# Kernel tuning notes

Measured on AMD Instinct MI355X. Metric: run time of the kernel, lower is better.

## Reference

```python
import jax, jax.numpy as jnp
import numpy as np

UNITS = 256


def setup_inputs() -> dict:
    key = jax.random.key(0)
    ks = jax.random.split(key, 9)
    B, H, W, C = 8, 64, 64, UNITS
    x = jax.random.normal(ks[0], (B, H, W, C), dtype=jnp.float32)
    # 1x1 Conv2D == per-pixel linear: weight [C_in, C_out], bias [C_out]
    def lin(k):
        return jax.random.normal(k, (C, UNITS), dtype=jnp.float32) * (2.0 / C) ** 0.5
    return {
        "x": x,
        "wq": lin(ks[1]), "bq": jnp.zeros((UNITS,), jnp.float32),
        "wk": lin(ks[2]), "bk": jnp.zeros((UNITS,), jnp.float32),
        "wv": lin(ks[3]), "bv": jnp.zeros((UNITS,), jnp.float32),
        "wp": lin(ks[4]), "bp": jnp.zeros((UNITS,), jnp.float32),
    }


def reference(x, wq, bq, wk, bk, wv, bv, wp, bp):
    B, H, W, C = x.shape
    N = H * W
    scale = jnp.asarray(UNITS, jnp.float32) ** -0.5
    xf = x.reshape(B, N, C)  # 1x1 conv == matmul over channels
    q = xf @ wq + bq
    k = xf @ wk + bk
    v = xf @ wv + bv
    # (b,h,w,c)x(b,H,W,c)->(b,h,w,H,W) flattened to (b,N,N)
    scores = jnp.einsum('bnc,bmc->bnm', q, k) * scale
    attn = jax.nn.softmax(scores, axis=-1)
    out = jnp.einsum('bnm,bmc->bnc', attn, v)
    proj = out @ wp + bp
    return x + proj.reshape(B, H, W, UNITS)
```

## Files before the change

### kernel.cpp

```cpp
#include <hip/hip_runtime.h>


typedef _Float16 half8 __attribute__((ext_vector_type(8)));
typedef _Float16 half4 __attribute__((ext_vector_type(4)));
typedef float f32x4 __attribute__((ext_vector_type(4)));
typedef float f32x16 __attribute__((ext_vector_type(16)));
typedef unsigned int u32x4 __attribute__((ext_vector_type(4)));
typedef unsigned int u32x2 __attribute__((ext_vector_type(2)));

#define MFMA16(a, b, c) __builtin_amdgcn_mfma_f32_16x16x32_f16((a), (b), (c), 0, 0, 0)
#define MFMA32(a, b, c) __builtin_amdgcn_mfma_f32_32x32x16_f16((a), (b), (c), 0, 0, 0)

#if __has_builtin(__builtin_amdgcn_exp2f)
#define EXP2(x) __builtin_amdgcn_exp2f(x)
#else
#define EXP2(x) exp2f(x)
#endif

#define QSCALE 0.09016843898f
#define ESHIFT 11.5415603f

__device__ __forceinline__ void lds_load16(const void* g, void* l) {
    __builtin_amdgcn_global_load_lds(
        (const __attribute__((address_space(1))) unsigned int*)g,
        (__attribute__((address_space(3))) unsigned int*)l, 16, 0, 0);
}

__global__ __launch_bounds__(256)
void wt_prep(const float* __restrict__ w0, const float* __restrict__ w1,
             const float* __restrict__ w2, const float* __restrict__ w3,
             _Float16* __restrict__ outw)
{
    __shared__ _Float16 sT[64 * 72];
    const int z = blockIdx.z;
    const float* W = (z == 0) ? w0 : (z == 1) ? w1 : (z == 2) ? w2 : w3;
    _Float16* O = outw + z * 65536;
    const int kb = blockIdx.x * 64, nb = blockIdx.y * 64;
    const int t = threadIdx.x;
    const int r = t >> 4, c4 = (t & 15) * 4;
#pragma unroll
    for (int i = 0; i < 4; ++i) {
        f32x4 ld = *(const f32x4*)(W + (size_t)(kb + r + i * 16) * 256 + nb + c4);
#pragma unroll
        for (int j = 0; j < 4; ++j) sT[(c4 + j) * 72 + r + i * 16] = (_Float16)ld[j];
    }
    __syncthreads();
#pragma unroll
    for (int i = 0; i < 4; ++i) {
        int n = r + i * 16;
        *(u32x2*)&O[(size_t)(nb + n) * 256 + kb + c4] = *(const u32x2*)&sT[n * 72 + c4];
    }
}

__global__ __launch_bounds__(256)
void qkv_gemm(const float* __restrict__ x, const _Float16* __restrict__ wt,
              const float* __restrict__ bq, const float* __restrict__ bk,
              const float* __restrict__ bv,
              _Float16* __restrict__ qo, _Float16* __restrict__ ko,
              _Float16* __restrict__ vo)
{
    __shared__ _Float16 smem[4 * 2560];
    _Float16* sA = smem;

    const int tid  = threadIdx.x;
    const int w    = tid >> 6;
    const int lane = tid & 63;
    const int quad = lane >> 4;
    const int l16  = lane & 15;
    const int m0   = blockIdx.x * 64;
    const int n0   = blockIdx.y * 64;
    const int rS = tid >> 2, cS = (tid & 3) << 3;

    const float* ap = x + (size_t)(m0 + rS) * 256 + cS;
    f32x4 a0 = *(const f32x4*)ap, a1 = *(const f32x4*)(ap + 4);
    u32x4 bst[3];
#pragma unroll
    for (int o = 0; o < 3; ++o)
        bst[o] = *(const u32x4*)(wt + o * 65536 + (size_t)(n0 + rS) * 256 + cS);

    f32x4 zero4 = {0.f, 0.f, 0.f, 0.f};
    f32x4 acc[3][4];
#pragma unroll
    for (int o = 0; o < 3; ++o)
#pragma unroll
        for (int mt = 0; mt < 4; ++mt) acc[o][mt] = zero4;

    for (int it = 0; it < 8; ++it) {
        __syncthreads();
        half8 t;
#pragma unroll
        for (int j = 0; j < 4; ++j) { t[j] = (_Float16)a0[j]; t[j + 4] = (_Float16)a1[j]; }
        *(half8*)&sA[rS * 40 + cS] = t;
#pragma unroll
        for (int o = 0; o < 3; ++o)
            *(u32x4*)&smem[2560 * (o + 1) + rS * 40 + cS] = bst[o];
        __syncthreads();
        if (it < 7) {
            int k0 = (it + 1) * 32;
            const float* ap2 = x + (size_t)(m0 + rS) * 256 + k0 + cS;
            a0 = *(const f32x4*)ap2; a1 = *(const f32x4*)(ap2 + 4);
#pragma unroll
            for (int o = 0; o < 3; ++o)
                bst[o] = *(const u32x4*)(wt + o * 65536 + (size_t)(n0 + rS) * 256 + k0 + cS);
        }
        half8 af[4];
#pragma unroll
        for (int mt = 0; mt < 4; ++mt)
            af[mt] = *(const half8*)&sA[(mt * 16 + l16) * 40 + quad * 8];
#pragma unroll
        for (int o = 0; o < 3; ++o) {
            half8 bf = *(const half8*)&smem[2560 * (o + 1) + (16 * w + l16) * 40 + quad * 8];
#pragma unroll
            for (int mt = 0; mt < 4; ++mt)
                acc[o][mt] = MFMA16(af[mt], bf, acc[o][mt]);
        }
    }

    const int col = n0 + 16 * w + l16;
#pragma unroll
    for (int mt = 0; mt < 4; ++mt) {
#pragma unroll
        for (int reg = 0; reg < 4; ++reg) {
            int row = m0 + 16 * mt + quad * 4 + reg;
            qo[(size_t)row * 256 + col] = (_Float16)((acc[0][mt][reg] + bq[col]) * QSCALE);
            ko[(size_t)row * 256 + col] = (_Float16)(acc[1][mt][reg] + bk[col]);
        }
    }
    __syncthreads();
    _Float16* sT = smem;
#pragma unroll
    for (int mt = 0; mt < 4; ++mt)
#pragma unroll
        for (int reg = 0; reg < 4; ++reg)
            sT[(16 * w + l16) * 72 + 16 * mt + quad * 4 + reg] =
                (_Float16)(acc[2][mt][reg] + bv[col]);
    __syncthreads();
    int ch = tid >> 2, po = (tid & 3) << 4;
    int bb = m0 >> 12, pix = m0 & 4095;
    _Float16* dst = vo + (size_t)bb * 1048576 + (size_t)(n0 + ch) * 4096 + pix + po;
    *(u32x4*)dst       = *(const u32x4*)&sT[ch * 72 + po];
    *(u32x4*)(dst + 8) = *(const u32x4*)&sT[ch * 72 + po + 8];
}

__global__ __launch_bounds__(256)
void proj_gemm(const _Float16* __restrict__ opart, const float* __restrict__ lpart,
               const _Float16* __restrict__ Wt, const float* __restrict__ bias,
               const float* __restrict__ resid, float* __restrict__ out)
{
    __shared__ _Float16 smem[2 * 2560];
    _Float16* sA = smem;
    _Float16* sB = smem + 2560;

    const int tid  = threadIdx.x;
    const int w    = tid >> 6;
    const int lane = tid & 63;
    const int quad = lane >> 4;
    const int l16  = lane & 15;
    const int m0   = blockIdx.x * 64;
    const int n0   = blockIdx.y * 64;
    const int rS = tid >> 2, cS = (tid & 3) << 3;

    const _Float16* o1p = opart;
    const _Float16* o2p = opart + 8388608;
    const int row = m0 + rS;
    const float inv = 1.0f / (lpart[row] + lpart[32768 + row]);

    u32x4 a1v = *(const u32x4*)(o1p + (size_t)row * 256 + cS);
    u32x4 a2v = *(const u32x4*)(o2p + (size_t)row * 256 + cS);
    u32x4 bst = *(const u32x4*)(Wt + (size_t)(n0 + rS) * 256 + cS);

    f32x4 zero4 = {0.f, 0.f, 0.f, 0.f};
    f32x4 acc[4] = {zero4, zero4, zero4, zero4};

    for (int it = 0; it < 8; ++it) {
        __syncthreads();
        {
            half8 h1 = *(half8*)&a1v, h2 = *(half8*)&a2v, t;
#pragma unroll
            for (int j = 0; j < 8; ++j)
                t[j] = (_Float16)(((float)h1[j] + (float)h2[j]) * inv);
            *(half8*)&sA[rS * 40 + cS] = t;
        }
        *(u32x4*)&sB[rS * 40 + cS] = bst;
        __syncthreads();
        if (it < 7) {
            int k0 = (it + 1) * 32;
            a1v = *(const u32x4*)(o1p + (size_t)row * 256 + k0 + cS);
            a2v = *(const u32x4*)(o2p + (size_t)row * 256 + k0 + cS);
            bst = *(const u32x4*)(Wt + (size_t)(n0 + rS) * 256 + k0 + cS);
        }
        half8 af = *(const half8*)&sA[(16 * w + l16) * 40 + quad * 8];
#pragma unroll
        for (int nt = 0; nt < 4; ++nt) {
            half8 bf = *(const half8*)&sB[(nt * 16 + l16) * 40 + quad * 8];
            acc[nt] = MFMA16(af, bf, acc[nt]);
        }
    }
#pragma unroll
    for (int nt = 0; nt < 4; ++nt) {
#pragma unroll
        for (int reg = 0; reg < 4; ++reg) {
            int orow = m0 + 16 * w + quad * 4 + reg;
            int col = n0 + nt * 16 + l16;
            out[(size_t)orow * 256 + col] =
                acc[nt][reg] + bias[col] + resid[(size_t)orow * 256 + col];
        }
    }
}

__global__ __launch_bounds__(256, 1)
void attn_kernel(const _Float16* __restrict__ q, const _Float16* __restrict__ k,
                 const _Float16* __restrict__ vt, _Float16* __restrict__ opart,
                 float* __restrict__ lpart)
{
    extern __shared__ char smem[];
    char* sKb = smem;
    char* sVb = smem + 32768;

    const int tid  = threadIdx.x;
    const int w    = tid >> 6;
    const int lane = tid & 63;
    const int l31  = lane & 31;
    const int hi   = lane >> 5;
    const int kh   = blockIdx.x & 1;
    const int qg   = (blockIdx.x >> 1) & 15;
    const int b    = blockIdx.x >> 5;

    char* sPw = smem + 65536 + w * 5120;

    const _Float16* kb = k  + (size_t)b * 1048576 + (size_t)kh * 524288;
    const _Float16* vb = vt + (size_t)b * 1048576 + kh * 2048;
    const int rowbase = qg * 256 + w * 64;

    half8 qf0[16], qf1[16];
    {
        const _Float16* q0 = q + (size_t)(b * 4096 + rowbase + l31) * 256 + hi * 8;
        const _Float16* q1 = q0 + 32 * 256;
#pragma unroll
        for (int s = 0; s < 16; ++s) {
            qf0[s] = *(const half8*)(q0 + s * 16);
            qf1[s] = *(const half8*)(q1 + s * 16);
        }
    }

    f32x16 o0[8], o1[8];
#pragma unroll
    for (int i = 0; i < 8; ++i)
#pragma unroll
        for (int j = 0; j < 16; ++j) { o0[i][j] = 0.f; o1[i][j] = 0.f; }
    float ls0 = 0.f, ls1 = 0.f;

    const int koffL = l31 * 256 + hi * 8;

#pragma unroll
    for (int j = 0; j < 4; ++j) {
        int s = w * 4 + j;
        lds_load16(kb + koffL + s * 16, sKb + s * 1024);
        int ct = s >> 1, ks = s & 1;
        lds_load16(vb + (size_t)(32 * ct + l31) * 4096 + 16 * ks + 8 * hi,
                   sVb + s * 1024);
    }

    for (int kt = 0; kt < 64; ++kt) {
        const int p = kt & 1;
        __syncthreads();

        if (kt < 63) {
            const _Float16* ktb = kb + (size_t)(kt + 1) * 8192;
            const _Float16* vtb = vb + (kt + 1) * 32;
            char* dK = sKb + (1 - p) * 16384;
            char* dV = sVb + (1 - p) * 16384;
#pragma unroll
            for (int j = 0; j < 4; ++j) {
                int s = w * 4 + j;
                lds_load16(ktb + koffL + s * 16, dK + s * 1024);
                int ct = s >> 1, ks = s & 1;
                lds_load16(vtb + (size_t)(32 * ct + l31) * 4096 + 16 * ks + 8 * hi,
                           dV + s * 1024);
            }
        }

        const char* K = sKb + p * 16384;
        const char* V = sVb + p * 16384;

        f32x16 sa0, sa1;
#pragma unroll
        for (int j = 0; j < 16; ++j) { sa0[j] = 0.f; sa1[j] = 0.f; }
#pragma unroll
        for (int s = 0; s < 16; ++s) {
            half8 af = *(const half8*)(K + s * 1024 + lane * 16);
            sa0 = MFMA32(af, qf0[s], sa0);
            sa1 = MFMA32(af, qf1[s], sa1);
        }

#pragma unroll
        for (int rb = 0; rb < 4; ++rb) {
            float p0 = EXP2(sa0[rb * 4 + 0] - ESHIFT);
            float p1 = EXP2(sa0[rb * 4 + 1] - ESHIFT);
            float p2 = EXP2(sa0[rb * 4 + 2] - ESHIFT);
            float p3 = EXP2(sa0[rb * 4 + 3] - ESHIFT);
            ls0 += (p0 + p1) + (p2 + p3);
            half4 t;
            t[0] = (_Float16)p0; t[1] = (_Float16)p1;
            t[2] = (_Float16)p2; t[3] = (_Float16)p3;
            *(half4*)(sPw + l31 * 80 + (8 * rb + 4 * hi) * 2) = t;

            float r0 = EXP2(sa1[rb * 4 + 0] - ESHIFT);
            float r1 = EXP2(sa1[rb * 4 + 1] - ESHIFT);
            float r2 = EXP2(sa1[rb * 4 + 2] - ESHIFT);
            float r3 = EXP2(sa1[rb * 4 + 3] - ESHIFT);
            ls1 += (r0 + r1) + (r2 + r3);
            half4 u;
            u[0] = (_Float16)r0; u[1] = (_Float16)r1;
            u[2] = (_Float16)r2; u[3] = (_Float16)r3;
            *(half4*)(sPw + (32 + l31) * 80 + (8 * rb + 4 * hi) * 2) = u;
        }
        __asm__ volatile("s_waitcnt lgkmcnt(0)" ::: "memory");
        half8 pf00 = *(const half8*)(sPw + l31 * 80 + hi * 16);
        half8 pf01 = *(const half8*)(sPw + l31 * 80 + 32 + hi * 16);
        half8 pf10 = *(const half8*)(sPw + (32 + l31) * 80 + hi * 16);
        half8 pf11 = *(const half8*)(sPw + (32 + l31) * 80 + 32 + hi * 16);

#pragma unroll
        for (int ct = 0; ct < 8; ++ct) {
            half8 b0 = *(const half8*)(V + (ct * 2 + 0) * 1024 + lane * 16);
            half8 b1 = *(const half8*)(V + (ct * 2 + 1) * 1024 + lane * 16);
            o0[ct] = MFMA32(pf00, b0, o0[ct]);
            o0[ct] = MFMA32(pf01, b1, o0[ct]);
            o1[ct] = MFMA32(pf10, b0, o1[ct]);
            o1[ct] = MFMA32(pf11, b1, o1[ct]);
        }
    }

    ls0 += __shfl_xor(ls0, 32);
    ls1 += __shfl_xor(ls1, 32);
    _Float16* po = opart + (size_t)kh * 8388608 + (size_t)(b * 4096 + rowbase) * 256;
    float* pl = lpart + kh * 32768 + b * 4096 + rowbase;
    if (hi == 0) { pl[l31] = ls0; pl[32 + l31] = ls1; }
#pragma unroll
    for (int ct = 0; ct < 8; ++ct) {
#pragma unroll
        for (int reg = 0; reg < 16; ++reg) {
            int row = (reg & 3) + 8 * (reg >> 2) + 4 * hi;
            po[(size_t)row * 256 + ct * 32 + l31] = (_Float16)o0[ct][reg];
            po[(size_t)(32 + row) * 256 + ct * 32 + l31] = (_Float16)o1[ct][reg];
        }
    }
}

extern "C" void kernel_launch(void* const* d_in, const int* in_sizes, int n_in,
                              void* d_out, int out_size, void* d_ws, size_t ws_size,
                              hipStream_t stream) {
    const float* x  = (const float*)d_in[0];
    const float* wq = (const float*)d_in[1];
    const float* bq = (const float*)d_in[2];
    const float* wk = (const float*)d_in[3];
    const float* bk = (const float*)d_in[4];
    const float* wv = (const float*)d_in[5];
    const float* bv = (const float*)d_in[6];
    const float* wp = (const float*)d_in[7];
    const float* bp = (const float*)d_in[8];

    _Float16* qws  = (_Float16*)d_ws;
    _Float16* kws  = qws + 8388608;
    _Float16* vtws = kws + 8388608;
    _Float16* ows  = vtws + 8388608;
    _Float16* wt   = ows + 16777216;
    float*    lws  = (float*)(wt + 262144);

    dim3 blk(256);

    (void)hipFuncSetAttribute((const void*)attn_kernel,
                              hipFuncAttributeMaxDynamicSharedMemorySize, 86016);

    wt_prep<<<dim3(4, 4, 4), blk, 0, stream>>>(wq, wk, wv, wp, wt);
    qkv_gemm<<<dim3(512, 4), blk, 0, stream>>>(x, wt, bq, bk, bv, qws, kws, vtws);
    attn_kernel<<<dim3(256), blk, 86016, stream>>>(qws, kws, vtws, ows, lws);
    proj_gemm<<<dim3(512, 4), blk, 0, stream>>>(ows, lws, wt + 196608, bp, x, (float*)d_out);
}
```

Before: 306.9 us.

## Split attention work across eight waves with 32 query rows each

Reworks the attention kernel so each block runs 512 threads (8 waves), each owning 32 query rows instead of 64. This halves the per-wave Q fragment, accumulator and P-tile state, aiming for more waves to hide latency. The QK^T reduction is also split across two independent accumulators to shorten the MFMA dependency chain. In exchange, each wave now reads the full K/V tiles from LDS for half as many rows, doubling LDS traffic per unit of work. The launch bound of (512,2) may also force a register cap tight enough to cause spills.

Result: faster. 290.7 us (-5.3%).

```diff
diff --git a/kernel.cpp b/kernel.cpp
--- a/kernel.cpp
+++ b/kernel.cpp
@@ -208,7 +208,7 @@
     }
 }
 
-__global__ __launch_bounds__(256, 1)
+__global__ __launch_bounds__(512, 2)
 void attn_kernel(const _Float16* __restrict__ q, const _Float16* __restrict__ k,
                  const _Float16* __restrict__ vt, _Float16* __restrict__ opart,
                  float* __restrict__ lpart)
@@ -226,35 +226,31 @@
     const int qg   = (blockIdx.x >> 1) & 15;
     const int b    = blockIdx.x >> 5;
 
-    char* sPw = smem + 65536 + w * 5120;
+    char* sPw = smem + 65536 + w * 2560;
 
     const _Float16* kb = k  + (size_t)b * 1048576 + (size_t)kh * 524288;
     const _Float16* vb = vt + (size_t)b * 1048576 + kh * 2048;
-    const int rowbase = qg * 256 + w * 64;
-
-    half8 qf0[16], qf1[16];
+    const int rowbase = qg * 256 + w * 32;
+
+    half8 qf[16];
     {
         const _Float16* q0 = q + (size_t)(b * 4096 + rowbase + l31) * 256 + hi * 8;
-        const _Float16* q1 = q0 + 32 * 256;
-#pragma unroll
-        for (int s = 0; s < 16; ++s) {
-            qf0[s] = *(const half8*)(q0 + s * 16);
-            qf1[s] = *(const half8*)(q1 + s * 16);
-        }
-    }
-
-    f32x16 o0[8], o1[8];
+#pragma unroll
+        for (int s = 0; s < 16; ++s) qf[s] = *(const half8*)(q0 + s * 16);
+    }
+
+    f32x16 o[8];
 #pragma unroll
     for (int i = 0; i < 8; ++i)
 #pragma unroll
-        for (int j = 0; j < 16; ++j) { o0[i][j] = 0.f; o1[i][j] = 0.f; }
-    float ls0 = 0.f, ls1 = 0.f;
+        for (int j = 0; j < 16; ++j) o[i][j] = 0.f;
+    float ls = 0.f;
 
     const int koffL = l31 * 256 + hi * 8;
 
 #pragma unroll
-    for (int j = 0; j < 4; ++j) {
-        int s = w * 4 + j;
+    for (int j = 0; j < 2; ++j) {
+        int s = w * 2 + j;
         lds_load16(kb + koffL + s * 16, sKb + s * 1024);
         int ct = s >> 1, ks = s & 1;
         lds_load16(vb + (size_t)(32 * ct + l31) * 4096 + 16 * ks + 8 * hi,
@@ -271,8 +267,8 @@
             char* dK = sKb + (1 - p) * 16384;
             char* dV = sVb + (1 - p) * 16384;
 #pragma unroll
-            for (int j = 0; j < 4; ++j) {
-                int s = w * 4 + j;
+            for (int j = 0; j < 2; ++j) {
+                int s = w * 2 + j;
                 lds_load16(ktb + koffL + s * 16, dK + s * 1024);
                 int ct = s >> 1, ks = s & 1;
                 lds_load16(vtb + (size_t)(32 * ct + l31) * 4096 + 16 * ks + 8 * hi,
@@ -283,67 +279,52 @@
         const char* K = sKb + p * 16384;
         const char* V = sVb + p * 16384;
 
-        f32x16 sa0, sa1;
-#pragma unroll
-        for (int j = 0; j < 16; ++j) { sa0[j] = 0.f; sa1[j] = 0.f; }
-#pragma unroll
-        for (int s = 0; s < 16; ++s) {
-            half8 af = *(const half8*)(K + s * 1024 + lane * 16);
-            sa0 = MFMA32(af, qf0[s], sa0);
-            sa1 = MFMA32(af, qf1[s], sa1);
+        f32x16 saA, saB;
+#pragma unroll
+        for (int j = 0; j < 16; ++j) { saA[j] = 0.f; saB[j] = 0.f; }
+#pragma unroll
+        for (int s = 0; s < 16; s += 2) {
+            half8 a0 = *(const half8*)(K + s * 1024 + lane * 16);
+            half8 a1 = *(const half8*)(K + (s + 1) * 1024 + lane * 16);
+            saA = MFMA32(a0, qf[s], saA);
+            saB = MFMA32(a1, qf[s + 1], saB);
         }
 
 #pragma unroll
         for (int rb = 0; rb < 4; ++rb) {
-            float p0 = EXP2(sa0[rb * 4 + 0] - ESHIFT);
-            float p1 = EXP2(sa0[rb * 4 + 1] - ESHIFT);
-            float p2 = EXP2(sa0[rb * 4 + 2] - ESHIFT);
-            float p3 = EXP2(sa0[rb * 4 + 3] - ESHIFT);
-            ls0 += (p0 + p1) + (p2 + p3);
+            float p0 = EXP2(saA[rb * 4 + 0] + saB[rb * 4 + 0] - ESHIFT);
+            float p1 = EXP2(saA[rb * 4 + 1] + saB[rb * 4 + 1] - ESHIFT);
+            float p2 = EXP2(saA[rb * 4 + 2] + saB[rb * 4 + 2] - ESHIFT);
+            float p3 = EXP2(saA[rb * 4 + 3] + saB[rb * 4 + 3] - ESHIFT);
+            ls += (p0 + p1) + (p2 + p3);
             half4 t;
             t[0] = (_Float16)p0; t[1] = (_Float16)p1;
             t[2] = (_Float16)p2; t[3] = (_Float16)p3;
             *(half4*)(sPw + l31 * 80 + (8 * rb + 4 * hi) * 2) = t;
-
-            float r0 = EXP2(sa1[rb * 4 + 0] - ESHIFT);
-            float r1 = EXP2(sa1[rb * 4 + 1] - ESHIFT);
-            float r2 = EXP2(sa1[rb * 4 + 2] - ESHIFT);
-            float r3 = EXP2(sa1[rb * 4 + 3] - ESHIFT);
-            ls1 += (r0 + r1) + (r2 + r3);
-            half4 u;
-            u[0] = (_Float16)r0; u[1] = (_Float16)r1;
-            u[2] = (_Float16)r2; u[3] = (_Float16)r3;
-            *(half4*)(sPw + (32 + l31) * 80 + (8 * rb + 4 * hi) * 2) = u;
         }
         __asm__ volatile("s_waitcnt lgkmcnt(0)" ::: "memory");
-        half8 pf00 = *(const half8*)(sPw + l31 * 80 + hi * 16);
-        half8 pf01 = *(const half8*)(sPw + l31 * 80 + 32 + hi * 16);
-        half8 pf10 = *(const half8*)(sPw + (32 + l31) * 80 + hi * 16);
-        half8 pf11 = *(const half8*)(sPw + (32 + l31) * 80 + 32 + hi * 16);
+        half8 pf0 = *(const half8*)(sPw + l31 * 80 + hi * 16);
+        half8 pf1 = *(const half8*)(sPw + l31 * 80 + 32 + hi * 16);
 
 #pragma unroll
         for (int ct = 0; ct < 8; ++ct) {
             half8 b0 = *(const half8*)(V + (ct * 2 + 0) * 1024 + lane * 16);
             half8 b1 = *(const half8*)(V + (ct * 2 + 1) * 1024 + lane * 16);
-            o0[ct] = MFMA32(pf00, b0, o0[ct]);
-            o0[ct] = MFMA32(pf01, b1, o0[ct]);
-            o1[ct] = MFMA32(pf10, b0, o1[ct]);
-            o1[ct] = MFMA32(pf11, b1, o1[ct]);
-        }
-    }
-
-    ls0 += __shfl_xor(ls0, 32);
-    ls1 += __shfl_xor(ls1, 32);
+            o[ct] = MFMA32(pf0, b0, o[ct]);
+            o[ct] = MFMA32(pf1, b1, o[ct]);
+        }
+    }
+
+    ls += __shfl_xor(ls, 32);
     _Float16* po = opart + (size_t)kh * 8388608 + (size_t)(b * 4096 + rowbase) * 256;
     float* pl = lpart + kh * 32768 + b * 4096 + rowbase;
-    if (hi == 0) { pl[l31] = ls0; pl[32 + l31] = ls1; }
+    if (hi == 0) pl[l31] = ls;
 #pragma unroll
     for (int ct = 0; ct < 8; ++ct) {
 #pragma unroll
         for (int reg = 0; reg < 16; ++reg) {
             int row = (reg & 3) + 8 * (reg >> 2) + 4 * hi;
-            po[(size_t)row * 256 + ct * 32 + l31] = (_Float16)o0[ct][reg];
-            po[(size_t)(32 + row) * 256 + ct * 32 + l31] = (_Float16)o1[ct][reg];
+            po[(size_t)row * 256 + ct * 32 + l31] = (_Float16)o[ct][reg];
         }
     }
 }
@@ -375,6 +356,6 @@
 
     wt_prep<<<dim3(4, 4, 4), blk, 0, stream>>>(wq, wk, wv, wp, wt);
     qkv_gemm<<<dim3(512, 4), blk, 0, stream>>>(x, wt, bq, bk, bv, qws, kws, vtws);
-    attn_kernel<<<dim3(256), blk, 86016, stream>>>(qws, kws, vtws, ows, lws);
+    attn_kernel<<<dim3(256), dim3(512), 86016, stream>>>(qws, kws, vtws, ows, lws);
     proj_gemm<<<dim3(512, 4), blk, 0, stream>>>(ows, lws, wt + 196608, bp, x, (float*)d_out);
 }
```
